# Kernel optimization log

Hardware: AMD Instinct MI355X
Metric: run time of the kernel (lower is better)

Reference implementation:

```python
import jax, jax.numpy as jnp
import numpy as np
from jax.scipy.special import logsumexp

WORD_DIM = 512
SCRF_DIM = 256
N_TAGS = 12
ALLOWED_SPAN = 8
START_ID = 10
STOP_ID = 11
SEQ_LEN = 768
N_SPANS = 96


def _compute_scores(h, Wl, bl, Wr, br, Gl, bgl, Gr, bgr, Wt, bt, transitions):
    # h: [1, L, D] already projected by Dense
    Lc, D = h.shape[1], h.shape[2]
    scores = jnp.zeros((1, Lc, Lc, D), h.dtype)
    diag = jnp.arange(Lc)
    ht = h
    scores = scores.at[:, diag, diag].set(ht)
    for sl in range(1, min(ALLOWED_SPAN, Lc)):
        l, r = ht[:, :-1], ht[:, 1:]
        h_hat = 4.0 * jax.nn.sigmoid(l @ Wl.T + bl + r @ Wr.T + br) - 2.0
        # exp/normalize over 3 gates == softmax over gate axis
        g = (l @ Gl.T + bgl + r @ Gr.T + bgr).reshape(1, Lc - sl, 3, D)
        wgt = jax.nn.softmax(g, axis=2)
        ht = wgt[:, :, 0] * h_hat + wgt[:, :, 1] * l + wgt[:, :, 2] * r
        scores = scores.at[:, diag[:Lc - sl], diag[sl:]].set(ht)
    tagsc = scores @ Wt.T + bt  # [1, L, L, T]
    # final[b,i,j,prev,tag] = tagsc[b,i,j,tag] + transitions[prev,tag]
    return tagsc[:, :, :, None, :] + transitions[None, None, None]


def _forward_pass(s5):
    # s5: [1, L, L, T, T]; semi-Markov forward algorithm, windows of width <= ALLOWED_SPAN
    Lc, T = s5.shape[1], s5.shape[3]
    A = ALLOWED_SPAN
    i0 = jnp.arange(1, Lc + 1)
    k = jnp.arange(A)
    p = i0[:, None] - A + k[None, :]              # candidate span-start positions [L, A]
    m = p >= 0                                    # valid window mask (istarts = max(0, i-A))
    x = s5[0][jnp.clip(p, 0), (i0 - 1)[:, None]]  # [L, A, T, T] span scores ending at i-1
    buf0 = jnp.full((A, T), -10000.0, s5.dtype).at[A - 1, START_ID].set(0.0)

    def step(buf, inp):
        xi, mi = inp
        # tmp[k, prev, tag] = score + logalpha[start, prev]
        tmp = jnp.where(mi[:, None, None], xi + buf[:, :, None], -1e30)
        na = logsumexp(tmp, axis=(0, 1))  # [T]
        return jnp.concatenate([buf[1:], na[None]], axis=0), na

    _, alphas = jax.lax.scan(step, buf0, (x, m))
    return alphas[-1, :STOP_ID].sum()


def _gold_score(s5, tags):
    Lc, T = s5.shape[1], s5.shape[3]
    gf = tags[:, :, 0] * (Lc * T * T) + tags[:, :, 1] * (T * T) + tags[:, :, 2] * T + tags[:, :, 3]
    return jnp.take_along_axis(s5.reshape(1, -1), gf, axis=1).sum()


def setup_inputs() -> dict:
    key = jax.random.key(0)
    ks = jax.random.split(key, 16)
    D, W3 = SCRF_DIM, 3 * SCRF_DIM
    s = 0.05
    def w(k, shape):
        return jax.random.normal(k, shape, dtype=jnp.float32) * s
    return {
        "feats": jax.random.normal(ks[0], (1, SEQ_LEN, WORD_DIM), dtype=jnp.float32),
        "tags": jax.random.randint(ks[1], (1, N_SPANS, 4), 0, N_TAGS),
        "Wd": w(ks[2], (D, WORD_DIM)), "bd": jnp.zeros((D,), jnp.float32),
        "Wl": w(ks[3], (D, D)), "bl": jnp.zeros((D,), jnp.float32),
        "Wr": w(ks[4], (D, D)), "br": jnp.zeros((D,), jnp.float32),
        "Gl": w(ks[5], (W3, D)), "bgl": jnp.zeros((W3,), jnp.float32),
        "Gr": w(ks[6], (W3, D)), "bgr": jnp.zeros((W3,), jnp.float32),
        "Wt": w(ks[7], (N_TAGS, D)), "bt": jnp.zeros((N_TAGS,), jnp.float32),
        "transitions": w(ks[8], (N_TAGS, N_TAGS)),
    }


def reference(feats, tags, Wd, bd, Wl, bl, Wr, br, Gl, bgl, Gr, bgr, Wt, bt, transitions):
    h = feats @ Wd.T + bd  # Dense: word_dim -> scrf_dim
    s5 = _compute_scores(h, Wl, bl, Wr, br, Gl, bgl, Gr, bgr, Wt, bt, transitions)
    gold = _gold_score(s5, tags)
    logZ = _forward_pass(s5)
    return logZ - gold
```

## Files before the change

kernel.cpp:

```cpp
#include <hip/hip_runtime.h>

typedef __attribute__((ext_vector_type(8))) short short8;
typedef __attribute__((ext_vector_type(4))) float f32x4;

#define TPAD 100

__device__ __forceinline__ float bf2f(short s) {
  return __uint_as_float(((unsigned)(unsigned short)s) << 16);
}
__device__ __forceinline__ unsigned short f2bf(float f) {
  unsigned u = __float_as_uint(f);
  unsigned rounding = 0x7fffu + ((u >> 16) & 1u);
  return (unsigned short)((u + rounding) >> 16);
}

struct F8 { float4 a, b; };
__device__ __forceinline__ F8 ldf8(const float* p) {
  F8 r; r.a = *(const float4*)p; r.b = *(const float4*)(p + 4); return r;
}
__device__ __forceinline__ short8 cvtF8(F8 v) {
  short8 r;
  r[0]=(short)f2bf(v.a.x); r[1]=(short)f2bf(v.a.y); r[2]=(short)f2bf(v.a.z); r[3]=(short)f2bf(v.a.w);
  r[4]=(short)f2bf(v.b.x); r[5]=(short)f2bf(v.b.y); r[6]=(short)f2bf(v.b.z); r[7]=(short)f2bf(v.b.w);
  return r;
}

__device__ __forceinline__ void stg_f32(float* p, float v) {
  asm volatile("global_store_dword %0, %1, off sc1" :: "v"(p), "v"(v) : "memory");
}
__device__ __forceinline__ void stg_u16(unsigned short* p, unsigned short v) {
  unsigned w = v;
  asm volatile("global_store_short %0, %1, off sc1" :: "v"(p), "v"(w) : "memory");
}
__device__ __forceinline__ void stg_u32(unsigned* p, unsigned v) {
  asm volatile("global_store_dword %0, %1, off sc1" :: "v"(p), "v"(v) : "memory");
}

#define NFLAGS 18432
__device__ __forceinline__ void flag_spin(unsigned* f, unsigned tgt) {
  unsigned n = 0;
  while (__hip_atomic_load(f, __ATOMIC_RELAXED, __HIP_MEMORY_SCOPE_AGENT) < tgt) {
    __builtin_amdgcn_s_sleep(1);
    if (++n > 2000000u) break;
  }
}
#define DRAIN() asm volatile("s_waitcnt vmcnt(0) lgkmcnt(0)" ::: "memory")
#define KTBAR() do { \
  asm volatile("s_waitcnt lgkmcnt(0)" ::: "memory"); \
  __builtin_amdgcn_s_barrier(); \
  __builtin_amdgcn_sched_barrier(0); \
} while (0)

union __align__(16) SmemU {
  struct { unsigned short As[2][64][72]; unsigned short Ws[2][64][72]; float Cs[64][64]; } g;
  struct { unsigned short As8[8][64][72]; float Cs[64][64]; } gi;
  struct { unsigned short rows[2][8][264]; float sred[2][96]; float smu[2]; } bn;
  struct { float Bs[96 * TPAD]; float Acs[96 * TPAD]; float red[8]; } t;
  struct { float Qs[2][96 * TPAD]; float vv[4][96]; float red[8]; float redm[4]; } f;
};

__global__ void prep_kernel(const float* __restrict__ bl, const float* __restrict__ br,
                            const float* __restrict__ bgl, const float* __restrict__ bgr,
                            float* __restrict__ bc, unsigned* __restrict__ flags)
{
  int idx = blockIdx.x * 256 + threadIdx.x;
  if (idx < 1024) {
    bc[idx] = (idx < 256) ? bl[idx] + br[idx] : bgl[idx-256] + bgr[idx-256];
  } else {
    int j = idx - 1024;
    if (j < NFLAGS) flags[j] = 0u;
  }
}

__device__ __forceinline__ void treelevel(SmemU& sm,
    const float* Tin, const float* Cin, float* Tout, float* Cout)
{
  const int bid = blockIdx.x;
  const int tid = threadIdx.x;
  const int wv = tid >> 6, lane = tid & 63;
  const int j = bid >> 1;
  const int cs = (bid & 1) * 48;
  const float* Ag = Tin + (size_t)(2*j) * 9216;
  const float* Bg = Tin + (size_t)(2*j + 1) * 9216;

  float4 av[9], bv[9];
  const float* ap = Ag + tid * 36;
  const float* bp = Bg + tid * 36;
  #pragma unroll
  for (int q = 0; q < 9; ++q) av[q] = *(const float4*)(ap + q*4);
  #pragma unroll
  for (int q = 0; q < 9; ++q) bv[q] = *(const float4*)(bp + q*4);
  float ma = 0.f, mb = 0.f;
  #pragma unroll
  for (int q = 0; q < 9; ++q) {
    ma = fmaxf(ma, fmaxf(fmaxf(av[q].x, av[q].y), fmaxf(av[q].z, av[q].w)));
    mb = fmaxf(mb, fmaxf(fmaxf(bv[q].x, bv[q].y), fmaxf(bv[q].z, bv[q].w)));
  }
  #pragma unroll
  for (int off = 32; off; off >>= 1) {
    ma = fmaxf(ma, __shfl_down(ma, off));
    mb = fmaxf(mb, __shfl_down(mb, off));
  }
  if (lane == 0) { sm.t.red[wv] = ma; sm.t.red[4 + wv] = mb; }
  __syncthreads();
  float fa = fmaxf(fmaxf(sm.t.red[0], sm.t.red[1]), fmaxf(sm.t.red[2], sm.t.red[3]));
  float fb = fmaxf(fmaxf(sm.t.red[4], sm.t.red[5]), fmaxf(sm.t.red[6], sm.t.red[7]));
  float ia = 1.0f / fa, ib = 1.0f / fb;

  #pragma unroll
  for (int q = 0; q < 9; ++q) {
    int e = tid*36 + q*4;
    int r = e / 96, k = e - r*96;
    float4 bb = bv[q];
    bb.x *= ib; bb.y *= ib; bb.z *= ib; bb.w *= ib;
    *(float4*)&sm.t.Bs[r*TPAD + k] = bb;
    float4 aa = av[q];
    sm.t.Acs[(k+0)*TPAD + r] = aa.x * ia;
    sm.t.Acs[(k+1)*TPAD + r] = aa.y * ia;
    sm.t.Acs[(k+2)*TPAD + r] = aa.z * ia;
    sm.t.Acs[(k+3)*TPAD + r] = aa.w * ia;
  }
  __syncthreads();

  int tr = tid >> 4, tc = tid & 15;
  int r0 = tr * 6, c0 = cs + tc * 3;
  float acc[6][3];
  #pragma unroll
  for (int i = 0; i < 6; ++i)
    #pragma unroll
    for (int m = 0; m < 3; ++m) acc[i][m] = 0.f;
  for (int k = 0; k < 96; k += 4) {
    float4 a0 = *(const float4*)&sm.t.Acs[(c0+0)*TPAD + k];
    float4 a1 = *(const float4*)&sm.t.Acs[(c0+1)*TPAD + k];
    float4 a2 = *(const float4*)&sm.t.Acs[(c0+2)*TPAD + k];
    #pragma unroll
    for (int i = 0; i < 6; ++i) {
      float4 b = *(const float4*)&sm.t.Bs[(r0+i)*TPAD + k];
      acc[i][0] += b.x*a0.x + b.y*a0.y + b.z*a0.z + b.w*a0.w;
      acc[i][1] += b.x*a1.x + b.y*a1.y + b.z*a1.z + b.w*a1.w;
      acc[i][2] += b.x*a2.x + b.y*a2.y + b.z*a2.z + b.w*a2.w;
    }
  }
  float* op = Tout + (size_t)j * 9216;
  #pragma unroll
  for (int i = 0; i < 6; ++i)
    #pragma unroll
    for (int m = 0; m < 3; ++m)
      stg_f32(&op[(size_t)(r0+i)*96 + c0 + m], acc[i][m]);
  if ((bid & 1) == 0 && tid == 0)
    stg_f32(&Cout[j], Cin[2*j] + Cin[2*j + 1] + __logf(fa) + __logf(fb));
}

__global__ __launch_bounds__(256, 1) void mega_kernel(
    const float* feats, const float* Wd, const float* bd,
    const float* Wl, const float* Wr, const float* Gl, const float* Gr,
    unsigned short* WcB, const float* bc,
    unsigned short* ht, const float* Wt, const float* bt,
    float* Bband, float* Xn, float* muv, const float* trans,
    const int* tags,
    float* T0, float* T1, float* T2, float* T3, float* T4,
    float* C0, float* C1, float* C2, float* C3, float* C4,
    float* out, unsigned* flags)
{
  __shared__ SmemU sm;
  const int bid = blockIdx.x;
  const int tid = threadIdx.x;
  const int wave = tid >> 6, lane = tid & 63;

  if (bid >= 48) {
    for (int j = (bid - 48)*256 + tid; j < 524288; j += 208*256) {
      int o = j >> 9, k = j & 511;
      float v;
      if (k < 256) v = (o < 256) ? Wl[o*256 + k] : Gl[(o-256)*256 + k];
      else { int k2 = k - 256; v = (o < 256) ? Wr[o*256 + k2] : Gr[(o-256)*256 + k2]; }
      stg_u16(&WcB[j], f2bf(v));
    }
    DRAIN();
    __syncthreads();
    if (tid == 0) atomicAdd(&flags[573*32], 1u);
  }

  if (bid < 192) {
    const int p = bid % 12;
    const int lr = tid >> 3;
    const int c8 = (tid & 7) * 8;
    if (bid < 48) {
      const int p0 = p * 64;
      const int n0 = (bid / 12) * 64;
      f32x4 acc[4];
      #pragma unroll
      for (int i = 0; i < 4; ++i)
        #pragma unroll
        for (int j = 0; j < 4; ++j) acc[i][j] = 0.f;
      F8 fa0[2], fa1[2], fw0[2], fw1[2];
      #pragma unroll
      for (int q = 0; q < 2; ++q) {
        int kb = q * 64;
        fa0[q] = ldf8(feats + (size_t)(p0 + lr)*512 + kb + c8);
        fa1[q] = ldf8(feats + (size_t)(p0 + lr + 32)*512 + kb + c8);
        fw0[q] = ldf8(Wd + (size_t)(n0 + lr)*512 + kb + c8);
        fw1[q] = ldf8(Wd + (size_t)(n0 + lr + 32)*512 + kb + c8);
      }
      #pragma unroll
      for (int kt = 0; kt < 8; ++kt) {
        const int sb = kt & 1;
        *(short8*)(&sm.g.As[sb][lr][c8])      = cvtF8(fa0[sb]);
        *(short8*)(&sm.g.As[sb][lr + 32][c8]) = cvtF8(fa1[sb]);
        *(short8*)(&sm.g.Ws[sb][lr][c8])      = cvtF8(fw0[sb]);
        *(short8*)(&sm.g.Ws[sb][lr + 32][c8]) = cvtF8(fw1[sb]);
        if (kt < 6) {
          int kb = (kt + 2) * 64;
          fa0[sb] = ldf8(feats + (size_t)(p0 + lr)*512 + kb + c8);
          fa1[sb] = ldf8(feats + (size_t)(p0 + lr + 32)*512 + kb + c8);
          fw0[sb] = ldf8(Wd + (size_t)(n0 + lr)*512 + kb + c8);
          fw1[sb] = ldf8(Wd + (size_t)(n0 + lr + 32)*512 + kb + c8);
        }
        KTBAR();
        int q8 = (lane >> 4) * 8;
        #pragma unroll
        for (int kk = 0; kk < 2; ++kk) {
          short8 bfr = *(const short8*)(&sm.g.Ws[sb][wave*16 + (lane & 15)][kk*32 + q8]);
          #pragma unroll
          for (int mt = 0; mt < 4; ++mt) {
            short8 afr = *(const short8*)(&sm.g.As[sb][mt*16 + (lane & 15)][kk*32 + q8]);
            acc[mt] = __builtin_amdgcn_mfma_f32_16x16x32_bf16(afr, bfr, acc[mt], 0, 0, 0);
          }
        }
        KTBAR();
      }
      int o = n0 + wave*16 + (lane & 15);
      float bias = bd[o];
      #pragma unroll
      for (int mt = 0; mt < 4; ++mt)
        #pragma unroll
        for (int r = 0; r < 4; ++r) {
          int row = p0 + mt*16 + (lane >> 4)*4 + r;
          stg_u16(&ht[row*256 + o], f2bf(acc[mt][r] + bias));
        }
      DRAIN();
      __syncthreads();
      if (tid == 0) atomicAdd(&flags[(0*12 + p)*32], 1u);
    }

    const int p0 = p * 64;
    const int n0i = (bid / 12) * 16;
    const int q8 = (lane >> 4) * 8;
    if (tid == 0) flag_spin(&flags[573*32], 208u);
    __syncthreads();
    short8 wfrag[16];
    {
      const size_t wrow = (size_t)(wave*256 + n0i + (lane & 15)) * 512;
      #pragma unroll
      for (int kt = 0; kt < 8; ++kt)
        #pragma unroll
        for (int kk = 0; kk < 2; ++kk)
          wfrag[kt*2 + kk] = *(const short8*)(WcB + wrow + kt*64 + kk*32 + q8);
    }
    for (int sl = 1; sl <= 7; ++sl) {
      unsigned tgt = (sl == 1) ? 4u : 16u;
      if (tid == 0) {
        flag_spin(&flags[((sl-1)*12 + p)*32], tgt);
        if (p < 11) flag_spin(&flags[((sl-1)*12 + p + 1)*32], tgt);
      }
      __syncthreads();
      const unsigned short* htp = ht + (size_t)(sl - 1) * 196608;
      unsigned short* htn = ht + (size_t)sl * 196608;
      const int Mvalid = 768 - sl;
      short8 areg[16];
      #pragma unroll
      for (int kt = 0; kt < 8; ++kt) {
        const int kcol = (kt & 3) * 64;
        const int shift = kt >> 2;
        int g0 = p0 + lr + shift;      if (g0 > 767) g0 = 767;
        int g1 = p0 + lr + 32 + shift; if (g1 > 767) g1 = 767;
        areg[kt*2]     = *(const short8*)(htp + (size_t)g0*256 + kcol + c8);
        areg[kt*2 + 1] = *(const short8*)(htp + (size_t)g1*256 + kcol + c8);
      }
      #pragma unroll
      for (int kt = 0; kt < 8; ++kt) {
        *(short8*)(&sm.gi.As8[kt][lr][c8])      = areg[kt*2];
        *(short8*)(&sm.gi.As8[kt][lr + 32][c8]) = areg[kt*2 + 1];
      }
      __syncthreads();
      f32x4 acc[4];
      #pragma unroll
      for (int i = 0; i < 4; ++i)
        #pragma unroll
        for (int j = 0; j < 4; ++j) acc[i][j] = 0.f;
      #pragma unroll
      for (int kt = 0; kt < 8; ++kt) {
        #pragma unroll
        for (int kk = 0; kk < 2; ++kk) {
          #pragma unroll
          for (int mt = 0; mt < 4; ++mt) {
            short8 afr = *(const short8*)(&sm.gi.As8[kt][mt*16 + (lane & 15)][kk*32 + q8]);
            acc[mt] = __builtin_amdgcn_mfma_f32_16x16x32_bf16(afr, wfrag[kt*2 + kk], acc[mt], 0, 0, 0);
          }
        }
      }
      #pragma unroll
      for (int mt = 0; mt < 4; ++mt)
        #pragma unroll
        for (int r = 0; r < 4; ++r)
          sm.gi.Cs[mt*16 + (lane >> 4)*4 + r][wave*16 + (lane & 15)] = acc[mt][r];
      __syncthreads();

      {
        int dl = tid & 7;
        int d0 = n0i + dl*2;
        int cc0 = dl*2;
        float bz0 = bc[d0],       bz1 = bc[d0+1];
        float b00 = bc[256 + d0], b01 = bc[256 + d0 + 1];
        float b10 = bc[512 + d0], b11 = bc[512 + d0 + 1];
        float b20 = bc[768 + d0], b21 = bc[768 + d0 + 1];
        for (int pr = tid >> 3; pr < 64; pr += 32) {
          int pw = p0 + pr;
          if (pw >= Mvalid) continue;
          float z0 = sm.gi.Cs[pr][cc0]      + bz0, z1 = sm.gi.Cs[pr][cc0+1]      + bz1;
          float g00 = sm.gi.Cs[pr][16+cc0]  + b00, g01 = sm.gi.Cs[pr][16+cc0+1]  + b01;
          float g10 = sm.gi.Cs[pr][32+cc0]  + b10, g11 = sm.gi.Cs[pr][32+cc0+1]  + b11;
          float g20 = sm.gi.Cs[pr][48+cc0]  + b20, g21 = sm.gi.Cs[pr][48+cc0+1]  + b21;
          unsigned lv = *(const unsigned*)(htp + (size_t)pw*256 + d0);
          unsigned rv = *(const unsigned*)(htp + (size_t)(pw+1)*256 + d0);
          float l0 = bf2f((short)(lv & 0xffff)), l1 = bf2f((short)(lv >> 16));
          float r0v = bf2f((short)(rv & 0xffff)), r1v = bf2f((short)(rv >> 16));
          float hh0 = 4.f / (1.f + __expf(-z0)) - 2.f;
          float hh1 = 4.f / (1.f + __expf(-z1)) - 2.f;
          float mg0 = fmaxf(g00, fmaxf(g10, g20));
          float mg1 = fmaxf(g01, fmaxf(g11, g21));
          float e00 = __expf(g00 - mg0), e10 = __expf(g10 - mg0), e20 = __expf(g20 - mg0);
          float e01 = __expf(g01 - mg1), e11 = __expf(g11 - mg1), e21 = __expf(g21 - mg1);
          float o0 = (e00*hh0 + e10*l0 + e20*r0v) / (e00 + e10 + e20);
          float o1 = (e01*hh1 + e11*l1 + e21*r1v) / (e01 + e11 + e21);
          unsigned pack = (unsigned)f2bf(o0) | ((unsigned)f2bf(o1) << 16);
          stg_u32((unsigned*)(htn + (size_t)pw*256 + d0), pack);
        }
      }
      DRAIN();
      __syncthreads();
      if (tid == 0) atomicAdd(&flags[(sl*12 + p)*32], 1u);
    }
  }

  for (int task = bid; task < 384; task += 256) {
    if (tid == 0) {
      int rlo = 2*task - 7; if (rlo < 0) rlo = 0;
      int tlo = rlo >> 6, thi = (2*task + 1) >> 6;
      flag_spin(&flags[(7*12 + tlo)*32], 16u);
      if (thi != tlo) flag_spin(&flags[(7*12 + thi)*32], 16u);
    }
    __syncthreads();
    const int half = tid >> 7;
    const int t2 = tid & 127;
    const int i = 2*task + 1 + half;
    for (int q = t2; q < 256; q += 128) {
      int k = q >> 5, cc = (q & 31) * 8;
      int pr = i - 8 + k;
      short8 v;
      if (pr >= 0) {
        int slx = 7 - k;
        v = *(const short8*)(ht + ((size_t)slx*768 + pr)*256 + cc);
      } else {
        #pragma unroll
        for (int j = 0; j < 8; ++j) v[j] = 0;
      }
      *(short8*)(&sm.bn.rows[half][k][cc]) = v;
    }
    __syncthreads();
    float res = -1e30f;
    if (t2 < 96) {
      int t = t2 >> 3, k = t2 & 7;
      int pr = i - 8 + k;
      if (pr >= 0) {
        float acc = 0.f;
        for (int dch = 0; dch < 256; dch += 8) {
          float4 wa = *(const float4*)(Wt + t*256 + dch);
          float4 wb = *(const float4*)(Wt + t*256 + dch + 4);
          short8 hv = *(const short8*)(&sm.bn.rows[half][k][dch]);
          acc += wa.x*bf2f(hv[0]) + wa.y*bf2f(hv[1]) + wa.z*bf2f(hv[2]) + wa.w*bf2f(hv[3])
               + wb.x*bf2f(hv[4]) + wb.y*bf2f(hv[5]) + wb.z*bf2f(hv[6]) + wb.w*bf2f(hv[7]);
        }
        res = acc + bt[t];
      }
      stg_f32(&Bband[(size_t)i*96 + t2], res);
      sm.bn.sred[half][t2] = res;
    }
    __syncthreads();
    if (t2 < 32) {
      float m = fmaxf(sm.bn.sred[half][t2],
                 fmaxf(sm.bn.sred[half][t2+32], sm.bn.sred[half][t2+64]));
      #pragma unroll
      for (int off = 16; off; off >>= 1) m = fmaxf(m, __shfl_down(m, off));
      if (t2 == 0) { stg_f32(&muv[i], m); sm.bn.smu[half] = m; }
    }
    __syncthreads();
    if (t2 < 96) stg_f32(&Xn[(size_t)i*96 + t2], __expf(res - sm.bn.smu[half]));
    DRAIN();
    __syncthreads();
    if (tid == 0) atomicAdd(&flags[(96 + task)*32], 1u);
  }
  if (bid >= 240) return;

  {
    const int chunk = bid / 5;
    const int bxx = bid % 5;
    if (tid == 0) {
      #pragma unroll
      for (int q = 0; q < 8; ++q)
        flag_spin(&flags[(96 + 8*chunk + q)*32], 1u);
    }
    __syncthreads();
    if (bxx == 0 && tid == 0) stg_f32(&C0[chunk], 0.f);
    const int a = chunk * 16;
    const int g = lane / 12;
    const int t = lane - g * 12;
    const int cidx = bxx * 20 + wave * 5 + g;
    const bool active = (g < 5) && (cidx < 96);
    const int c = active ? cidx : 95;
    const int s = c / 12, tau = c - s * 12;
    float Etc[12];
    #pragma unroll
    for (int jj = 0; jj < 12; ++jj) Etc[jj] = __expf(trans[jj*12 + t]);
    float NA[8], V[8];
    #pragma unroll
    for (int jj = 0; jj < 8; ++jj) { NA[jj] = 0.f; V[jj] = 0.f; }
    #pragma unroll
    for (int jj = 0; jj < 8; ++jj) if (jj == s) {
      NA[jj] = (t == tau) ? 1.f : 0.f;
      V[jj]  = Etc[tau];
    }
    const int gbb = (g * 12) * 4;
    #pragma unroll
    for (int m = 1; m <= 16; ++m) {
      const float* xr = Xn + (size_t)(a + m) * 96 + t * 8;
      float4 x0 = *(const float4*)xr;
      float4 x1 = *(const float4*)(xr + 4);
      float sf = __expf(-muv[a + m]);
      float na = x0.x*V[0] + x0.y*V[1] + x0.z*V[2] + x0.w*V[3]
               + x1.x*V[4] + x1.y*V[5] + x1.z*V[6] + x1.w*V[7];
      int nai = __float_as_int(na);
      float nb[12];
      #pragma unroll
      for (int jj = 0; jj < 12; ++jj)
        nb[jj] = __int_as_float(__builtin_amdgcn_ds_bpermute(gbb + jj*4, nai));
      float pp0 = nb[0]*Etc[0] + nb[1]*Etc[1] + nb[2]*Etc[2]   + nb[3]*Etc[3];
      float pp1 = nb[4]*Etc[4] + nb[5]*Etc[5] + nb[6]*Etc[6]   + nb[7]*Etc[7];
      float pp2 = nb[8]*Etc[8] + nb[9]*Etc[9] + nb[10]*Etc[10] + nb[11]*Etc[11];
      float v = (pp0 + pp1) + pp2;
      #pragma unroll
      for (int kq = 0; kq < 7; ++kq) { NA[kq] = NA[kq+1]*sf; V[kq] = V[kq+1]*sf; }
      NA[7] = na; V[7] = v;
    }
    if (active) {
      float* dst = T0 + (size_t)chunk * 9216 + c;
      #pragma unroll
      for (int jj = 0; jj < 8; ++jj) stg_f32(&dst[(size_t)(jj*12 + t) * 96], NA[jj]);
    }
    DRAIN();
    __syncthreads();
    if (tid == 0) atomicAdd(&flags[(480 + chunk)*32], 1u);
  }
  if (bid >= 48) return;

  {
    int j = bid >> 1;
    if (tid == 0) {
      flag_spin(&flags[(480 + 2*j    )*32], 5u);
      flag_spin(&flags[(480 + 2*j + 1)*32], 5u);
    }
    __syncthreads();
    treelevel(sm, T0, C0, T1, C1);
    DRAIN(); __syncthreads();
    if (tid == 0) atomicAdd(&flags[(528 + j)*32], 1u);
  }
  if (bid >= 24) return;
  {
    int j = bid >> 1;
    if (tid == 0) {
      flag_spin(&flags[(528 + 2*j    )*32], 2u);
      flag_spin(&flags[(528 + 2*j + 1)*32], 2u);
    }
    __syncthreads();
    treelevel(sm, T1, C1, T2, C2);
    DRAIN(); __syncthreads();
    if (tid == 0) atomicAdd(&flags[(552 + j)*32], 1u);
  }
  if (bid >= 12) return;
  {
    int j = bid >> 1;
    if (tid == 0) {
      flag_spin(&flags[(552 + 2*j    )*32], 2u);
      flag_spin(&flags[(552 + 2*j + 1)*32], 2u);
    }
    __syncthreads();
    treelevel(sm, T2, C2, T3, C3);
    DRAIN(); __syncthreads();
    if (tid == 0) atomicAdd(&flags[(564 + j)*32], 1u);
  }
  if (bid >= 6) return;
  {
    int j = bid >> 1;
    if (tid == 0) {
      flag_spin(&flags[(564 + 2*j    )*32], 2u);
      flag_spin(&flags[(564 + 2*j + 1)*32], 2u);
    }
    __syncthreads();
    treelevel(sm, T3, C3, T4, C4);
    DRAIN(); __syncthreads();
    if (tid == 0) atomicAdd(&flags[(570 + j)*32], 1u);
  }
  if (bid) return;

  {
    if (tid == 0) {
      flag_spin(&flags[(570)*32], 2u);
      flag_spin(&flags[(571)*32], 2u);
      flag_spin(&flags[(572)*32], 2u);
    }
    __syncthreads();
    float4 P[9];
    const float* p0p = T4 + tid * 36;
    #pragma unroll
    for (int q = 0; q < 9; ++q) P[q] = *(const float4*)(p0p + q*4);

    float gold = 0.f;
    if (tid < 96) {
      int a = tags[tid*4+0], b = tags[tid*4+1], cc = tags[tid*4+2], d = tags[tid*4+3];
      float v = trans[cc*12 + d];
      int sl = b - a;
      if (sl >= 0 && sl < 8) v += Bband[(size_t)(b+1)*96 + d*8 + (7 - sl)];
      else v += bt[d];
      gold = v;
    }
    float mp = 0.f;
    for (int q = tid; q < 768; q += 256) mp += muv[1 + q];
    #pragma unroll
    for (int off = 32; off; off >>= 1) {
      gold += __shfl_down(gold, off);
      mp   += __shfl_down(mp, off);
    }
    if (lane == 0) { sm.f.red[wave] = gold; sm.f.red[4 + wave] = mp; }

    #pragma unroll
    for (int q = 0; q < 9; ++q) {
      int e = tid*36 + q*4;
      int r = e / 96, k = e - r*96;
      *(float4*)&sm.f.Qs[0][r*TPAD + k] = P[q];
    }
    if (tid < 96) sm.f.vv[0][tid] = (tid == 94) ? 1.f : 0.f;
    __syncthreads();
    float gold_t = sm.f.red[0] + sm.f.red[1] + sm.f.red[2] + sm.f.red[3];
    float musum  = sm.f.red[4] + sm.f.red[5] + sm.f.red[6] + sm.f.red[7];
    float Ct = C4[0] + C4[1] + C4[2];

    #pragma unroll
    for (int s = 0; s < 3; ++s) {
      if (s < 2) {
        const float* pn = T4 + (size_t)(s+1)*9216 + tid*36;
        #pragma unroll
        for (int q = 0; q < 9; ++q) P[q] = *(const float4*)(pn + q*4);
      }
      float acc = 0.f;
      if (tid < 96) {
        const float* Qr = &sm.f.Qs[s & 1][tid * TPAD];
        #pragma unroll
        for (int k = 0; k < 96; k += 4) {
          float4 qv = *(const float4*)(Qr + k);
          float4 zv = *(const float4*)&sm.f.vv[s][k];
          acc += qv.x*zv.x + qv.y*zv.y + qv.z*zv.z + qv.w*zv.w;
        }
      }
      float am = (tid < 96) ? acc : 0.f;
      #pragma unroll
      for (int off = 32; off; off >>= 1) am = fmaxf(am, __shfl_down(am, off));
      if (lane == 0) sm.f.redm[wave] = am;
      __syncthreads();
      float mx = fmaxf(fmaxf(sm.f.redm[0], sm.f.redm[1]), fmaxf(sm.f.redm[2], sm.f.redm[3]));
      Ct += __logf(mx);
      if (tid < 96) sm.f.vv[s+1][tid] = acc / mx;
      if (s < 2) {
        #pragma unroll
        for (int q = 0; q < 9; ++q) {
          int e = tid*36 + q*4;
          int r = e / 96, k = e - r*96;
          *(float4*)&sm.f.Qs[(s+1)&1][r*TPAD + k] = P[q];
        }
      }
      __syncthreads();
    }
    if (tid == 0) {
      float lsum = 0.f;
      #pragma unroll
      for (int t = 0; t < 11; ++t) lsum += __logf(sm.f.vv[3][84 + t]);
      out[0] = lsum + 11.f * (Ct + musum) - gold_t;
    }
  }
}

extern "C" void kernel_launch(void* const* d_in, const int* in_sizes, int n_in,
                              void* d_out, int out_size, void* d_ws, size_t ws_size,
                              hipStream_t stream)
{
  const float* feats = (const float*)d_in[0];
  const int*   tags  = (const int*)  d_in[1];
  const float* Wd    = (const float*)d_in[2];
  const float* bd    = (const float*)d_in[3];
  const float* Wl    = (const float*)d_in[4];
  const float* bl    = (const float*)d_in[5];
  const float* Wr    = (const float*)d_in[6];
  const float* br    = (const float*)d_in[7];
  const float* Gl    = (const float*)d_in[8];
  const float* bgl   = (const float*)d_in[9];
  const float* Gr    = (const float*)d_in[10];
  const float* bgr   = (const float*)d_in[11];
  const float* Wt    = (const float*)d_in[12];
  const float* bt    = (const float*)d_in[13];
  const float* trans = (const float*)d_in[14];
  float* out = (float*)d_out;

  char* ws = (char*)d_ws;
  unsigned short* WcB    = (unsigned short*)(ws + 1048576);
  float*          bc     = (float*)         (ws + 2097152);
  unsigned short* ht     = (unsigned short*)(ws + 2101248);
  float*          Bband  = (float*)         (ws + 5246976);
  float*          Xn     = (float*)         (ws + 5542272);
  float*          muv    = (float*)         (ws + 5837568);
  float*          T0     = (float*)         (ws + 5841664);
  float*          T1     = (float*)         (ws + 7611136);
  float*          T2     = (float*)         (ws + 8495872);
  float*          T3     = (float*)         (ws + 8938240);
  float*          T4     = (float*)         (ws + 9159424);
  float*          C0     = (float*)         (ws + 9270016);
  float*          C1     = (float*)         (ws + 9270272);
  float*          C2     = (float*)         (ws + 9270528);
  float*          C3     = (float*)         (ws + 9270784);
  float*          C4     = (float*)         (ws + 9271040);
  unsigned*       flags  = (unsigned*)      (ws + 9271296);

  prep_kernel<<<76, 256, 0, stream>>>(bl, br, bgl, bgr, bc, flags);
  mega_kernel<<<256, 256, 0, stream>>>(feats, Wd, bd, Wl, Wr, Gl, Gr, WcB, bc,
                                       ht, Wt, bt, Bband, Xn, muv, trans, tags,
                                       T0, T1, T2, T3, T4, C0, C1, C2, C3, C4,
                                       out, flags);
}
```

Measured before the change: 193.3 us.

## Consolidate span recurrence onto 48 blocks with 64-wide column tiles

The span-combination recurrence used to be split across 192 blocks, each owning 16 output columns. It now runs on 48 blocks, each owning 64 columns: every wave holds four weight fragment sets, issues 4x the MFMAs and writes a 4-slab C tile. This cuts the number of blocks that sync through global flags per step and the redundant A-tile loads. In exchange there is more serial work per block, high register pressure from 64 short8 weight fragments plus 16 accumulators, and a larger LDS footprint.

Measured after the change: 256.1 us. 32.5% more time.

```diff
diff --git a/kernel.cpp b/kernel.cpp
--- a/kernel.cpp
+++ b/kernel.cpp
@@ -53,7 +53,7 @@
 
 union __align__(16) SmemU {
   struct { unsigned short As[2][64][72]; unsigned short Ws[2][64][72]; float Cs[64][64]; } g;
-  struct { unsigned short As8[8][64][72]; float Cs[64][64]; } gi;
+  struct { unsigned short As8[8][64][72]; float Cs4[4][64][64]; } gi;
   struct { unsigned short rows[2][8][264]; float sred[2][96]; float smu[2]; } bn;
   struct { float Bs[96 * TPAD]; float Acs[96 * TPAD]; float red[8]; } t;
   struct { float Qs[2][96 * TPAD]; float vv[4][96]; float red[8]; float redm[4]; } f;
@@ -180,13 +180,16 @@
     if (tid == 0) atomicAdd(&flags[573*32], 1u);
   }
 
-  if (bid < 192) {
+  if (bid < 48) {
     const int p = bid % 12;
+    const int nb = bid / 12;
+    const int d0b = nb * 64;
     const int lr = tid >> 3;
     const int c8 = (tid & 7) * 8;
-    if (bid < 48) {
+    const int q8 = (lane >> 4) * 8;
+    {
       const int p0 = p * 64;
-      const int n0 = (bid / 12) * 64;
+      const int n0 = nb * 64;
       f32x4 acc[4];
       #pragma unroll
       for (int i = 0; i < 4; ++i)
@@ -216,7 +219,6 @@
           fw1[sb] = ldf8(Wd + (size_t)(n0 + lr + 32)*512 + kb + c8);
         }
         KTBAR();
-        int q8 = (lane >> 4) * 8;
         #pragma unroll
         for (int kk = 0; kk < 2; ++kk) {
           short8 bfr = *(const short8*)(&sm.g.Ws[sb][wave*16 + (lane & 15)][kk*32 + q8]);
@@ -243,24 +245,22 @@
     }
 
     const int p0 = p * 64;
-    const int n0i = (bid / 12) * 16;
-    const int q8 = (lane >> 4) * 8;
     if (tid == 0) flag_spin(&flags[573*32], 208u);
     __syncthreads();
-    short8 wfrag[16];
-    {
-      const size_t wrow = (size_t)(wave*256 + n0i + (lane & 15)) * 512;
+    short8 wfrag[64];
+    #pragma unroll
+    for (int nt = 0; nt < 4; ++nt) {
+      const size_t wrow = (size_t)(wave*256 + d0b + nt*16 + (lane & 15)) * 512;
       #pragma unroll
       for (int kt = 0; kt < 8; ++kt)
         #pragma unroll
         for (int kk = 0; kk < 2; ++kk)
-          wfrag[kt*2 + kk] = *(const short8*)(WcB + wrow + kt*64 + kk*32 + q8);
+          wfrag[nt*16 + kt*2 + kk] = *(const short8*)(WcB + wrow + kt*64 + kk*32 + q8);
     }
     for (int sl = 1; sl <= 7; ++sl) {
-      unsigned tgt = (sl == 1) ? 4u : 16u;
       if (tid == 0) {
-        flag_spin(&flags[((sl-1)*12 + p)*32], tgt);
-        if (p < 11) flag_spin(&flags[((sl-1)*12 + p + 1)*32], tgt);
+        flag_spin(&flags[((sl-1)*12 + p)*32], 4u);
+        if (p < 11) flag_spin(&flags[((sl-1)*12 + p + 1)*32], 4u);
       }
       __syncthreads();
       const unsigned short* htp = ht + (size_t)(sl - 1) * 196608;
@@ -282,11 +282,13 @@
         *(short8*)(&sm.gi.As8[kt][lr + 32][c8]) = areg[kt*2 + 1];
       }
       __syncthreads();
-      f32x4 acc[4];
+      f32x4 acc[4][4];
       #pragma unroll
       for (int i = 0; i < 4; ++i)
         #pragma unroll
-        for (int j = 0; j < 4; ++j) acc[i][j] = 0.f;
+        for (int j = 0; j < 4; ++j)
+          #pragma unroll
+          for (int e = 0; e < 4; ++e) acc[i][j][e] = 0.f;
       #pragma unroll
       for (int kt = 0; kt < 8; ++kt) {
         #pragma unroll
@@ -294,32 +296,37 @@
           #pragma unroll
           for (int mt = 0; mt < 4; ++mt) {
             short8 afr = *(const short8*)(&sm.gi.As8[kt][mt*16 + (lane & 15)][kk*32 + q8]);
-            acc[mt] = __builtin_amdgcn_mfma_f32_16x16x32_bf16(afr, wfrag[kt*2 + kk], acc[mt], 0, 0, 0);
+            #pragma unroll
+            for (int nt = 0; nt < 4; ++nt)
+              acc[mt][nt] = __builtin_amdgcn_mfma_f32_16x16x32_bf16(afr, wfrag[nt*16 + kt*2 + kk], acc[mt][nt], 0, 0, 0);
           }
         }
       }
       #pragma unroll
       for (int mt = 0; mt < 4; ++mt)
         #pragma unroll
-        for (int r = 0; r < 4; ++r)
-          sm.gi.Cs[mt*16 + (lane >> 4)*4 + r][wave*16 + (lane & 15)] = acc[mt][r];
+        for (int nt = 0; nt < 4; ++nt)
+          #pragma unroll
+          for (int r = 0; r < 4; ++r)
+            sm.gi.Cs4[wave][mt*16 + (lane >> 4)*4 + r][nt*16 + (lane & 15)] = acc[mt][nt][r];
       __syncthreads();
 
       {
-        int dl = tid & 7;
-        int d0 = n0i + dl*2;
-        int cc0 = dl*2;
+        int dl = (tid & 31) * 2;
+        int d0 = d0b + dl;
         float bz0 = bc[d0],       bz1 = bc[d0+1];
         float b00 = bc[256 + d0], b01 = bc[256 + d0 + 1];
         float b10 = bc[512 + d0], b11 = bc[512 + d0 + 1];
         float b20 = bc[768 + d0], b21 = bc[768 + d0 + 1];
-        for (int pr = tid >> 3; pr < 64; pr += 32) {
+        #pragma unroll
+        for (int pq = 0; pq < 8; ++pq) {
+          int pr = (tid >> 5) + pq * 8;
           int pw = p0 + pr;
           if (pw >= Mvalid) continue;
-          float z0 = sm.gi.Cs[pr][cc0]      + bz0, z1 = sm.gi.Cs[pr][cc0+1]      + bz1;
-          float g00 = sm.gi.Cs[pr][16+cc0]  + b00, g01 = sm.gi.Cs[pr][16+cc0+1]  + b01;
-          float g10 = sm.gi.Cs[pr][32+cc0]  + b10, g11 = sm.gi.Cs[pr][32+cc0+1]  + b11;
-          float g20 = sm.gi.Cs[pr][48+cc0]  + b20, g21 = sm.gi.Cs[pr][48+cc0+1]  + b21;
+          float z0  = sm.gi.Cs4[0][pr][dl]   + bz0, z1  = sm.gi.Cs4[0][pr][dl+1] + bz1;
+          float g00 = sm.gi.Cs4[1][pr][dl]   + b00, g01 = sm.gi.Cs4[1][pr][dl+1] + b01;
+          float g10 = sm.gi.Cs4[2][pr][dl]   + b10, g11 = sm.gi.Cs4[2][pr][dl+1] + b11;
+          float g20 = sm.gi.Cs4[3][pr][dl]   + b20, g21 = sm.gi.Cs4[3][pr][dl+1] + b21;
           unsigned lv = *(const unsigned*)(htp + (size_t)pw*256 + d0);
           unsigned rv = *(const unsigned*)(htp + (size_t)(pw+1)*256 + d0);
           float l0 = bf2f((short)(lv & 0xffff)), l1 = bf2f((short)(lv >> 16));
@@ -346,8 +353,8 @@
     if (tid == 0) {
       int rlo = 2*task - 7; if (rlo < 0) rlo = 0;
       int tlo = rlo >> 6, thi = (2*task + 1) >> 6;
-      flag_spin(&flags[(7*12 + tlo)*32], 16u);
-      if (thi != tlo) flag_spin(&flags[(7*12 + thi)*32], 16u);
+      flag_spin(&flags[(7*12 + tlo)*32], 4u);
+      if (thi != tlo) flag_spin(&flags[(7*12 + thi)*32], 4u);
     }
     __syncthreads();
     const int half = tid >> 7;
```

## Refine inter-block flag dependencies and spin on multiple flags in parallel

Applied to the files above, without the earlier changes.

The band-scoring stage now handles one row per task with its own completion flag, so downstream chunks wait on finer-grained dependencies instead of paired rows. In the span recurrence, the current-tile half of the inputs is loaded and staged before the block waits on the neighbouring tile's flag, overlapping that wait with useful work. Multiple flag waits are spread across separate threads instead of serialised in thread 0. The flag array grows and the prep kernel gets more blocks to clear it, and per-row tasks mean more barriers and atomics overall.

After: 193.0 us, median of 2. About the same (-0.2%).

```diff
diff --git a/kernel.cpp b/kernel.cpp
--- a/kernel.cpp
+++ b/kernel.cpp
@@ -36,7 +36,7 @@
   asm volatile("global_store_dword %0, %1, off sc1" :: "v"(p), "v"(v) : "memory");
 }
 
-#define NFLAGS 18432
+#define NFLAGS 30688
 __device__ __forceinline__ void flag_spin(unsigned* f, unsigned tgt) {
   unsigned n = 0;
   while (__hip_atomic_load(f, __ATOMIC_RELAXED, __HIP_MEMORY_SCOPE_AGENT) < tgt) {
@@ -54,7 +54,7 @@
 union __align__(16) SmemU {
   struct { unsigned short As[2][64][72]; unsigned short Ws[2][64][72]; float Cs[64][64]; } g;
   struct { unsigned short As8[8][64][72]; float Cs[64][64]; } gi;
-  struct { unsigned short rows[2][8][264]; float sred[2][96]; float smu[2]; } bn;
+  struct { unsigned short rows[8][264]; float sred[96]; float smu; } bn;
   struct { float Bs[96 * TPAD]; float Acs[96 * TPAD]; float red[8]; } t;
   struct { float Qs[2][96 * TPAD]; float vv[4][96]; float red[8]; float redm[4]; } f;
 };
@@ -177,13 +177,14 @@
     }
     DRAIN();
     __syncthreads();
-    if (tid == 0) atomicAdd(&flags[573*32], 1u);
+    if (tid == 0) atomicAdd(&flags[958*32], 1u);
   }
 
   if (bid < 192) {
     const int p = bid % 12;
     const int lr = tid >> 3;
     const int c8 = (tid & 7) * 8;
+    const int q8 = (lane >> 4) * 8;
     if (bid < 48) {
       const int p0 = p * 64;
       const int n0 = (bid / 12) * 64;
@@ -216,7 +217,6 @@
           fw1[sb] = ldf8(Wd + (size_t)(n0 + lr + 32)*512 + kb + c8);
         }
         KTBAR();
-        int q8 = (lane >> 4) * 8;
         #pragma unroll
         for (int kk = 0; kk < 2; ++kk) {
           short8 bfr = *(const short8*)(&sm.g.Ws[sb][wave*16 + (lane & 15)][kk*32 + q8]);
@@ -244,8 +244,7 @@
 
     const int p0 = p * 64;
     const int n0i = (bid / 12) * 16;
-    const int q8 = (lane >> 4) * 8;
-    if (tid == 0) flag_spin(&flags[573*32], 208u);
+    if (tid == 0) flag_spin(&flags[958*32], 208u);
     __syncthreads();
     short8 wfrag[16];
     {
@@ -258,26 +257,35 @@
     }
     for (int sl = 1; sl <= 7; ++sl) {
       unsigned tgt = (sl == 1) ? 4u : 16u;
-      if (tid == 0) {
-        flag_spin(&flags[((sl-1)*12 + p)*32], tgt);
-        if (p < 11) flag_spin(&flags[((sl-1)*12 + p + 1)*32], tgt);
-      }
+      if (tid == 0) flag_spin(&flags[((sl-1)*12 + p)*32], tgt);
       __syncthreads();
       const unsigned short* htp = ht + (size_t)(sl - 1) * 196608;
       unsigned short* htn = ht + (size_t)sl * 196608;
       const int Mvalid = 768 - sl;
       short8 areg[16];
       #pragma unroll
-      for (int kt = 0; kt < 8; ++kt) {
+      for (int kt = 0; kt < 4; ++kt) {
+        const int kcol = kt * 64;
+        areg[kt*2]     = *(const short8*)(htp + (size_t)(p0 + lr)*256 + kcol + c8);
+        areg[kt*2 + 1] = *(const short8*)(htp + (size_t)(p0 + lr + 32)*256 + kcol + c8);
+      }
+      if (tid == 64 && p < 11) flag_spin(&flags[((sl-1)*12 + p + 1)*32], tgt);
+      #pragma unroll
+      for (int kt = 0; kt < 4; ++kt) {
+        *(short8*)(&sm.gi.As8[kt][lr][c8])      = areg[kt*2];
+        *(short8*)(&sm.gi.As8[kt][lr + 32][c8]) = areg[kt*2 + 1];
+      }
+      __syncthreads();
+      #pragma unroll
+      for (int kt = 4; kt < 8; ++kt) {
         const int kcol = (kt & 3) * 64;
-        const int shift = kt >> 2;
-        int g0 = p0 + lr + shift;      if (g0 > 767) g0 = 767;
-        int g1 = p0 + lr + 32 + shift; if (g1 > 767) g1 = 767;
+        int g0 = p0 + lr + 1;      if (g0 > 767) g0 = 767;
+        int g1 = p0 + lr + 33;     if (g1 > 767) g1 = 767;
         areg[kt*2]     = *(const short8*)(htp + (size_t)g0*256 + kcol + c8);
         areg[kt*2 + 1] = *(const short8*)(htp + (size_t)g1*256 + kcol + c8);
       }
       #pragma unroll
-      for (int kt = 0; kt < 8; ++kt) {
+      for (int kt = 4; kt < 8; ++kt) {
         *(short8*)(&sm.gi.As8[kt][lr][c8])      = areg[kt*2];
         *(short8*)(&sm.gi.As8[kt][lr + 32][c8]) = areg[kt*2 + 1];
       }
@@ -342,19 +350,17 @@
     }
   }
 
-  for (int task = bid; task < 384; task += 256) {
-    if (tid == 0) {
-      int rlo = 2*task - 7; if (rlo < 0) rlo = 0;
-      int tlo = rlo >> 6, thi = (2*task + 1) >> 6;
-      flag_spin(&flags[(7*12 + tlo)*32], 16u);
-      if (thi != tlo) flag_spin(&flags[(7*12 + thi)*32], 16u);
-    }
-    __syncthreads();
-    const int half = tid >> 7;
-    const int t2 = tid & 127;
-    const int i = 2*task + 1 + half;
-    for (int q = t2; q < 256; q += 128) {
-      int k = q >> 5, cc = (q & 31) * 8;
+  for (int i1 = bid; i1 < 768; i1 += 256) {
+    const int i = i1 + 1;
+    if (tid < 2) {
+      int rlo = i - 8; if (rlo < 0) rlo = 0;
+      int tlo = rlo >> 6, thi = (i - 1) >> 6;
+      int tt = (tid == 0) ? tlo : thi;
+      flag_spin(&flags[(7*12 + tt)*32], 16u);
+    }
+    __syncthreads();
+    {
+      int k = tid >> 5, cc = (tid & 31) * 8;
       int pr = i - 8 + k;
       short8 v;
       if (pr >= 0) {
@@ -364,51 +370,46 @@
         #pragma unroll
         for (int j = 0; j < 8; ++j) v[j] = 0;
       }
-      *(short8*)(&sm.bn.rows[half][k][cc]) = v;
+      *(short8*)(&sm.bn.rows[k][cc]) = v;
     }
     __syncthreads();
     float res = -1e30f;
-    if (t2 < 96) {
-      int t = t2 >> 3, k = t2 & 7;
+    if (tid < 96) {
+      int t = tid >> 3, k = tid & 7;
       int pr = i - 8 + k;
       if (pr >= 0) {
         float acc = 0.f;
         for (int dch = 0; dch < 256; dch += 8) {
           float4 wa = *(const float4*)(Wt + t*256 + dch);
           float4 wb = *(const float4*)(Wt + t*256 + dch + 4);
-          short8 hv = *(const short8*)(&sm.bn.rows[half][k][dch]);
+          short8 hv = *(const short8*)(&sm.bn.rows[k][dch]);
           acc += wa.x*bf2f(hv[0]) + wa.y*bf2f(hv[1]) + wa.z*bf2f(hv[2]) + wa.w*bf2f(hv[3])
                + wb.x*bf2f(hv[4]) + wb.y*bf2f(hv[5]) + wb.z*bf2f(hv[6]) + wb.w*bf2f(hv[7]);
         }
         res = acc + bt[t];
       }
-      stg_f32(&Bband[(size_t)i*96 + t2], res);
-      sm.bn.sred[half][t2] = res;
-    }
-    __syncthreads();
-    if (t2 < 32) {
-      float m = fmaxf(sm.bn.sred[half][t2],
-                 fmaxf(sm.bn.sred[half][t2+32], sm.bn.sred[half][t2+64]));
+      stg_f32(&Bband[(size_t)i*96 + tid], res);
+      sm.bn.sred[tid] = res;
+    }
+    __syncthreads();
+    if (tid < 32) {
+      float m = fmaxf(sm.bn.sred[tid], fmaxf(sm.bn.sred[tid+32], sm.bn.sred[tid+64]));
       #pragma unroll
       for (int off = 16; off; off >>= 1) m = fmaxf(m, __shfl_down(m, off));
-      if (t2 == 0) { stg_f32(&muv[i], m); sm.bn.smu[half] = m; }
-    }
-    __syncthreads();
-    if (t2 < 96) stg_f32(&Xn[(size_t)i*96 + t2], __expf(res - sm.bn.smu[half]));
+      if (tid == 0) { stg_f32(&muv[i], m); sm.bn.smu = m; }
+    }
+    __syncthreads();
+    if (tid < 96) stg_f32(&Xn[(size_t)i*96 + tid], __expf(res - sm.bn.smu));
     DRAIN();
     __syncthreads();
-    if (tid == 0) atomicAdd(&flags[(96 + task)*32], 1u);
+    if (tid == 0) atomicAdd(&flags[(96 + i1)*32], 1u);
   }
   if (bid >= 240) return;
 
   {
     const int chunk = bid / 5;
     const int bxx = bid % 5;
-    if (tid == 0) {
-      #pragma unroll
-      for (int q = 0; q < 8; ++q)
-        flag_spin(&flags[(96 + 8*chunk + q)*32], 1u);
-    }
+    if (tid < 16) flag_spin(&flags[(96 + 16*chunk + tid)*32], 1u);
     __syncthreads();
     if (bxx == 0 && tid == 0) stg_f32(&C0[chunk], 0.f);
     const int a = chunk * 16;
@@ -458,65 +459,49 @@
     }
     DRAIN();
     __syncthreads();
-    if (tid == 0) atomicAdd(&flags[(480 + chunk)*32], 1u);
+    if (tid == 0) atomicAdd(&flags[(864 + chunk)*32], 1u);
   }
   if (bid >= 48) return;
 
   {
     int j = bid >> 1;
-    if (tid == 0) {
-      flag_spin(&flags[(480 + 2*j    )*32], 5u);
-      flag_spin(&flags[(480 + 2*j + 1)*32], 5u);
-    }
+    if (tid < 2) flag_spin(&flags[(864 + 2*j + tid)*32], 5u);
     __syncthreads();
     treelevel(sm, T0, C0, T1, C1);
     DRAIN(); __syncthreads();
-    if (tid == 0) atomicAdd(&flags[(528 + j)*32], 1u);
+    if (tid == 0) atomicAdd(&flags[(912 + j)*32], 1u);
   }
   if (bid >= 24) return;
   {
     int j = bid >> 1;
-    if (tid == 0) {
-      flag_spin(&flags[(528 + 2*j    )*32], 2u);
-      flag_spin(&flags[(528 + 2*j + 1)*32], 2u);
-    }
+    if (tid < 2) flag_spin(&flags[(912 + 2*j + tid)*32], 2u);
     __syncthreads();
     treelevel(sm, T1, C1, T2, C2);
     DRAIN(); __syncthreads();
-    if (tid == 0) atomicAdd(&flags[(552 + j)*32], 1u);
+    if (tid == 0) atomicAdd(&flags[(936 + j)*32], 1u);
   }
   if (bid >= 12) return;
   {
     int j = bid >> 1;
-    if (tid == 0) {
-      flag_spin(&flags[(552 + 2*j    )*32], 2u);
-      flag_spin(&flags[(552 + 2*j + 1)*32], 2u);
-    }
+    if (tid < 2) flag_spin(&flags[(936 + 2*j + tid)*32], 2u);
     __syncthreads();
     treelevel(sm, T2, C2, T3, C3);
     DRAIN(); __syncthreads();
-    if (tid == 0) atomicAdd(&flags[(564 + j)*32], 1u);
+    if (tid == 0) atomicAdd(&flags[(948 + j)*32], 1u);
   }
   if (bid >= 6) return;
   {
     int j = bid >> 1;
-    if (tid == 0) {
-      flag_spin(&flags[(564 + 2*j    )*32], 2u);
-      flag_spin(&flags[(564 + 2*j + 1)*32], 2u);
-    }
+    if (tid < 2) flag_spin(&flags[(948 + 2*j + tid)*32], 2u);
     __syncthreads();
     treelevel(sm, T3, C3, T4, C4);
     DRAIN(); __syncthreads();
-    if (tid == 0) atomicAdd(&flags[(570 + j)*32], 1u);
+    if (tid == 0) atomicAdd(&flags[(954 + j)*32], 1u);
   }
   if (bid) return;
 
   {
-    if (tid == 0) {
-      flag_spin(&flags[(570)*32], 2u);
-      flag_spin(&flags[(571)*32], 2u);
-      flag_spin(&flags[(572)*32], 2u);
-    }
+    if (tid < 3) flag_spin(&flags[(954 + tid)*32], 2u);
     __syncthreads();
     float4 P[9];
     const float* p0p = T4 + tid * 36;
@@ -637,7 +622,7 @@
   float*          C4     = (float*)         (ws + 9271040);
   unsigned*       flags  = (unsigned*)      (ws + 9271296);
 
-  prep_kernel<<<76, 256, 0, stream>>>(bl, br, bgl, bgr, bc, flags);
+  prep_kernel<<<124, 256, 0, stream>>>(bl, br, bgl, bgr, bc, flags);
   mega_kernel<<<256, 256, 0, stream>>>(feats, Wd, bd, Wl, Wr, Gl, Gr, WcB, bc,
                                        ht, Wt, bt, Bband, Xn, muv, trans, tags,
                                        T0, T1, T2, T3, T4, C0, C1, C2, C3, C4,
```
